# Kernel tuning notes

Hardware: AMD Instinct MI355X
Metric: run time of the kernel (lower is better)

The kernel has to match this reference:

```python
import jax, jax.numpy as jnp
import numpy as np

IN_CH = 256
OUT_CH = 128
N = 6144
ADJ_P = 0.01  # edge density -> avg degree ~61


def setup_inputs() -> dict:
    key = jax.random.key(0)
    ks = jax.random.split(key, 8)
    x = jax.random.normal(ks[0], (1, IN_CH, N), dtype=jnp.float32)
    adj = (jax.random.uniform(ks[1], (N, N)) < ADJ_P).astype(jnp.float32)
    W_fts = jax.random.normal(ks[2], (OUT_CH, IN_CH), dtype=jnp.float32) * 0.05
    w1 = jax.random.normal(ks[3], (OUT_CH,), dtype=jnp.float32) * 0.05
    b1 = jnp.zeros((1,), dtype=jnp.float32)
    w2 = jax.random.normal(ks[4], (OUT_CH,), dtype=jnp.float32) * 0.05
    b2 = jnp.zeros((1,), dtype=jnp.float32)
    vars_bias = jax.random.normal(ks[5], (1, N, OUT_CH), dtype=jnp.float32) * 0.02
    return {"x": x, "adj": adj, "W_fts": W_fts, "w1": w1, "b1": b1,
            "w2": w2, "b2": b2, "vars_bias": vars_bias}


def reference(x, adj, W_fts, w1, b1, w2, b2, vars_bias):
    # fts = Conv1d(in, out, k=1, bias=False)(x): [1, OUT_CH, N]
    fts = jnp.einsum('oi,bin->bon', W_fts, x)
    f = fts[0]  # [OUT_CH, N]
    # f1/f2 = Conv1d(out, 1, 1)(fts) -> per-node scalars [N]
    f1 = jnp.einsum('o,on->n', w1, f) + b1  # [N]
    f2 = jnp.einsum('o,on->n', w2, f) + b2  # [N]
    # scores[i,j] = leaky_relu(adj[i,j]*f1[i] + adj[i,j]*f2[j], 0.2)
    scores = jax.nn.leaky_relu(adj * f1[:, None] + adj * f2[None, :], 0.2)
    # sparse_softmax2d: per-row softmax masked to nonzero entries
    mask = (scores != 0).astype(scores.dtype)
    m = jnp.max(scores, axis=1, keepdims=True)  # stabilizer; cancels in ratio
    exps = jnp.exp(scores - m) * mask
    coefs = exps / jnp.sum(exps, axis=1, keepdims=True)  # [N, N]
    # vals = coefs @ fts.T : [N, OUT_CH]
    vals = coefs @ f.T
    # add bias, permute to [1, OUT_CH, N]
    ret = jnp.transpose(vals[None, :, :] + vars_bias, (0, 2, 1))
    return ret
```

## Files before the change

kernel.cpp:

```cpp
#include <hip/hip_runtime.h>

#define NN  6144
#define ICH 256
#define OCH 128
#define WPB 4
#define NWIN 6
#define QCAP 256

__global__ __launch_bounds__(256) void k_fts(const float* __restrict__ x,
        const float* __restrict__ W, const float* __restrict__ w1,
        const float* __restrict__ w2, float* __restrict__ ft,
        float* __restrict__ f1, float* __restrict__ f2) {
    __shared__ float xs[32][32];
    __shared__ float Ws[32][OCH + 4];
    const int n0  = blockIdx.x * 32;
    const int tid = threadIdx.x;
    const int oq = (tid & 31) * 4;
    const int nq = (tid >> 5) * 4;
    float acc[4][4] = {};
    for (int k0 = 0; k0 < ICH; k0 += 32) {
        __syncthreads();
        {
            const int nn = tid & 31;
            const int kb = tid >> 5;
#pragma unroll
            for (int r = 0; r < 4; ++r)
                xs[kb + r * 8][nn] = x[(size_t)(k0 + kb + r * 8) * NN + n0 + nn];
        }
        {
            const int kk = tid & 31;
            const int ob = tid >> 5;
#pragma unroll
            for (int r = 0; r < 16; ++r) {
                const int o = ob + r * 8;
                Ws[kk][o] = W[o * ICH + k0 + kk];
            }
        }
        __syncthreads();
#pragma unroll
        for (int kk = 0; kk < 32; ++kk) {
            const float4 xv = *(const float4*)&xs[kk][nq];
            const float4 wv = *(const float4*)&Ws[kk][oq];
            const float xa[4] = {xv.x, xv.y, xv.z, xv.w};
            const float wa[4] = {wv.x, wv.y, wv.z, wv.w};
#pragma unroll
            for (int a = 0; a < 4; ++a)
#pragma unroll
                for (int b = 0; b < 4; ++b)
                    acc[a][b] = fmaf(xa[a], wa[b], acc[a][b]);
        }
    }
#pragma unroll
    for (int a = 0; a < 4; ++a) {
        float4 v = make_float4(acc[a][0], acc[a][1], acc[a][2], acc[a][3]);
        *(float4*)&ft[(size_t)(n0 + nq + a) * OCH + oq] = v;
    }
    const float4 w1v = *(const float4*)(w1 + oq);
    const float4 w2v = *(const float4*)(w2 + oq);
    float p1[4], p2[4];
#pragma unroll
    for (int a = 0; a < 4; ++a) {
        p1[a] = acc[a][0] * w1v.x + acc[a][1] * w1v.y + acc[a][2] * w1v.z + acc[a][3] * w1v.w;
        p2[a] = acc[a][0] * w2v.x + acc[a][1] * w2v.y + acc[a][2] * w2v.z + acc[a][3] * w2v.w;
    }
#pragma unroll
    for (int m = 16; m > 0; m >>= 1) {
#pragma unroll
        for (int a = 0; a < 4; ++a) {
            p1[a] += __shfl_xor(p1[a], m);
            p2[a] += __shfl_xor(p2[a], m);
        }
    }
    if ((tid & 31) == 0) {
#pragma unroll
        for (int a = 0; a < 4; ++a) {
            f1[n0 + nq + a] = p1[a];
            f2[n0 + nq + a] = p2[a];
        }
    }
}

__global__ __launch_bounds__(256) void k_attn(const float* __restrict__ adj,
        const float* __restrict__ ft, const float* __restrict__ f1,
        const float* __restrict__ f2, const float* __restrict__ b1,
        const float* __restrict__ b2, const float* __restrict__ vb,
        float* __restrict__ out) {
    __shared__ float q_e[QCAP];
    __shared__ int   q_j[QCAP];
    __shared__ int   cnt;
    __shared__ float dpart[WPB];
    __shared__ float part[WPB][OCH];
    const int tid  = threadIdx.x;
    const int lane = tid & 63;
    const int wave = tid >> 6;
    const int i = blockIdx.x;
    if (tid == 0) cnt = 0;
    __syncthreads();
    const float s1 = f1[i] + b1[0] + b2[0];
    const float* arow = adj + (size_t)i * NN;
    const int jbase = wave * (NN / WPB) + lane * 4;
    float4 a[NWIN];
#pragma unroll
    for (int w = 0; w < NWIN; ++w)
        a[w] = *(const float4*)(arow + jbase + w * 256);
    float den = 0.f;
#pragma unroll
    for (int w = 0; w < NWIN; ++w) {
        const float4 a4 = a[w];
        const int j0 = jbase + w * 256;
        const int k = (a4.x != 0.f) + (a4.y != 0.f) + (a4.z != 0.f) + (a4.w != 0.f);
        if (k) {
            const float4 g = *(const float4*)(f2 + j0);
            int slot = atomicAdd(&cnt, k);
            if (slot + k <= QCAP) {
                if (a4.x != 0.f) { float s = s1 + g.x; s = s > 0.f ? s : 0.2f * s;
                                   float e = __expf(s); den += e; q_j[slot] = j0;     q_e[slot] = e; ++slot; }
                if (a4.y != 0.f) { float s = s1 + g.y; s = s > 0.f ? s : 0.2f * s;
                                   float e = __expf(s); den += e; q_j[slot] = j0 + 1; q_e[slot] = e; ++slot; }
                if (a4.z != 0.f) { float s = s1 + g.z; s = s > 0.f ? s : 0.2f * s;
                                   float e = __expf(s); den += e; q_j[slot] = j0 + 2; q_e[slot] = e; ++slot; }
                if (a4.w != 0.f) { float s = s1 + g.w; s = s > 0.f ? s : 0.2f * s;
                                   float e = __expf(s); den += e; q_j[slot] = j0 + 3; q_e[slot] = e; }
            }
        }
    }
#pragma unroll
    for (int off = 32; off > 0; off >>= 1) den += __shfl_xor(den, off);
    if (lane == 0) dpart[wave] = den;
    __syncthreads();
    const int nE = cnt < QCAP ? cnt : QCAP;
    float2 nm = make_float2(0.f, 0.f);
    const int c0 = 2 * lane;
    for (int idx = wave; idx < nE; idx += WPB) {
        const int   j = q_j[idx];
        const float e = q_e[idx];
        const float2 g = *(const float2*)(ft + (size_t)j * OCH + c0);
        nm.x = fmaf(e, g.x, nm.x);
        nm.y = fmaf(e, g.y, nm.y);
    }
    part[wave][c0]     = nm.x;
    part[wave][c0 + 1] = nm.y;
    __syncthreads();
    if (tid < OCH) {
        const float d   = dpart[0] + dpart[1] + dpart[2] + dpart[3];
        const float inv = 1.f / d;
        const float v = part[0][tid] + part[1][tid] + part[2][tid] + part[3][tid];
        out[(size_t)tid * NN + i] = fmaf(v, inv, vb[(size_t)i * OCH + tid]);
    }
}

extern "C" void kernel_launch(void* const* d_in, const int* in_sizes, int n_in,
                              void* d_out, int out_size, void* d_ws, size_t ws_size,
                              hipStream_t stream) {
    const float* x   = (const float*)d_in[0];
    const float* adj = (const float*)d_in[1];
    const float* W   = (const float*)d_in[2];
    const float* w1  = (const float*)d_in[3];
    const float* b1  = (const float*)d_in[4];
    const float* w2  = (const float*)d_in[5];
    const float* b2  = (const float*)d_in[6];
    const float* vb  = (const float*)d_in[7];
    float* out = (float*)d_out;

    char* ws = (char*)d_ws;
    float* ft = (float*)ws;
    float* f1 = (float*)(ws + 3145728);
    float* f2 = (float*)(ws + 3145728 + 24576);

    k_fts<<<dim3(NN / 32), 256, 0, stream>>>(x, W, w1, w2, ft, f1, f2);
    k_attn<<<dim3(NN), 256, 0, stream>>>(adj, ft, f1, f2, b1, b2, vb, out);
}
```

Baseline: 272.3 us.

## Assign one adjacency row per wavefront with double-buffered nontemporal loads

The attention kernel now maps one row to each 64-lane wavefront, so a 256-thread block covers four rows, instead of one row per block. This removes block-wide barriers and the cross-wave partial reductions. Adjacency loads are nontemporal and double-buffered in 1536-element chunks to keep more memory traffic in flight. The gather now uses float4 over two half-waves joined by a shuffle. The per-row edge queue capacity drops to 160, which could silently drop edges on denser rows. The uncoalesced transposed output stores remain.

```diff
diff --git a/kernel.cpp b/kernel.cpp
--- a/kernel.cpp
+++ b/kernel.cpp
@@ -3,9 +3,9 @@
 #define NN  6144
 #define ICH 256
 #define OCH 128
-#define WPB 4
-#define NWIN 6
-#define QCAP 256
+#define QW  160
+
+typedef float vf4 __attribute__((ext_vector_type(4)));
 
 __global__ __launch_bounds__(256) void k_fts(const float* __restrict__ x,
         const float* __restrict__ W, const float* __restrict__ w1,
@@ -85,67 +85,81 @@
         const float* __restrict__ f2, const float* __restrict__ b1,
         const float* __restrict__ b2, const float* __restrict__ vb,
         float* __restrict__ out) {
-    __shared__ float q_e[QCAP];
-    __shared__ int   q_j[QCAP];
-    __shared__ int   cnt;
-    __shared__ float dpart[WPB];
-    __shared__ float part[WPB][OCH];
+    __shared__ float q_e[4][QW];
+    __shared__ int   q_j[4][QW];
+    __shared__ int   qc[4];
     const int tid  = threadIdx.x;
     const int lane = tid & 63;
     const int wave = tid >> 6;
-    const int i = blockIdx.x;
-    if (tid == 0) cnt = 0;
-    __syncthreads();
+    const int i = blockIdx.x * 4 + wave;
+    if (lane == 0) qc[wave] = 0;
     const float s1 = f1[i] + b1[0] + b2[0];
     const float* arow = adj + (size_t)i * NN;
-    const int jbase = wave * (NN / WPB) + lane * 4;
-    float4 a[NWIN];
+    float den = 0.f;
+    vf4 ab[2][6];
 #pragma unroll
-    for (int w = 0; w < NWIN; ++w)
-        a[w] = *(const float4*)(arow + jbase + w * 256);
-    float den = 0.f;
+    for (int w = 0; w < 6; ++w)
+        ab[0][w] = __builtin_nontemporal_load((const vf4*)(arow + lane * 4 + w * 256));
 #pragma unroll
-    for (int w = 0; w < NWIN; ++w) {
-        const float4 a4 = a[w];
-        const int j0 = jbase + w * 256;
-        const int k = (a4.x != 0.f) + (a4.y != 0.f) + (a4.z != 0.f) + (a4.w != 0.f);
-        if (k) {
-            const float4 g = *(const float4*)(f2 + j0);
-            int slot = atomicAdd(&cnt, k);
-            if (slot + k <= QCAP) {
-                if (a4.x != 0.f) { float s = s1 + g.x; s = s > 0.f ? s : 0.2f * s;
-                                   float e = __expf(s); den += e; q_j[slot] = j0;     q_e[slot] = e; ++slot; }
-                if (a4.y != 0.f) { float s = s1 + g.y; s = s > 0.f ? s : 0.2f * s;
-                                   float e = __expf(s); den += e; q_j[slot] = j0 + 1; q_e[slot] = e; ++slot; }
-                if (a4.z != 0.f) { float s = s1 + g.z; s = s > 0.f ? s : 0.2f * s;
-                                   float e = __expf(s); den += e; q_j[slot] = j0 + 2; q_e[slot] = e; ++slot; }
-                if (a4.w != 0.f) { float s = s1 + g.w; s = s > 0.f ? s : 0.2f * s;
-                                   float e = __expf(s); den += e; q_j[slot] = j0 + 3; q_e[slot] = e; }
+    for (int b = 0; b < 4; ++b) {
+        if (b < 3) {
+#pragma unroll
+            for (int w = 0; w < 6; ++w)
+                ab[(b + 1) & 1][w] = __builtin_nontemporal_load(
+                    (const vf4*)(arow + (b + 1) * 1536 + lane * 4 + w * 256));
+        }
+#pragma unroll
+        for (int w = 0; w < 6; ++w) {
+            const vf4 a4 = ab[b & 1][w];
+            const int j0 = b * 1536 + w * 256 + lane * 4;
+            const int k = (a4.x != 0.f) + (a4.y != 0.f) + (a4.z != 0.f) + (a4.w != 0.f);
+            if (k) {
+                const float4 g = *(const float4*)(f2 + j0);
+                int slot = atomicAdd(&qc[wave], k);
+                if (slot + k <= QW) {
+                    if (a4.x != 0.f) { float s = s1 + g.x; s = s > 0.f ? s : 0.2f * s;
+                                       float e = __expf(s); den += e;
+                                       q_j[wave][slot] = j0;     q_e[wave][slot] = e; ++slot; }
+                    if (a4.y != 0.f) { float s = s1 + g.y; s = s > 0.f ? s : 0.2f * s;
+                                       float e = __expf(s); den += e;
+                                       q_j[wave][slot] = j0 + 1; q_e[wave][slot] = e; ++slot; }
+                    if (a4.z != 0.f) { float s = s1 + g.z; s = s > 0.f ? s : 0.2f * s;
+                                       float e = __expf(s); den += e;
+                                       q_j[wave][slot] = j0 + 2; q_e[wave][slot] = e; ++slot; }
+                    if (a4.w != 0.f) { float s = s1 + g.w; s = s > 0.f ? s : 0.2f * s;
+                                       float e = __expf(s); den += e;
+                                       q_j[wave][slot] = j0 + 3; q_e[wave][slot] = e; }
+                }
             }
         }
     }
 #pragma unroll
     for (int off = 32; off > 0; off >>= 1) den += __shfl_xor(den, off);
-    if (lane == 0) dpart[wave] = den;
-    __syncthreads();
-    const int nE = cnt < QCAP ? cnt : QCAP;
-    float2 nm = make_float2(0.f, 0.f);
-    const int c0 = 2 * lane;
-    for (int idx = wave; idx < nE; idx += WPB) {
-        const int   j = q_j[idx];
-        const float e = q_e[idx];
-        const float2 g = *(const float2*)(ft + (size_t)j * OCH + c0);
+    const float inv = 1.f / den;
+    const int nE = qc[wave] < QW ? qc[wave] : QW;
+    const int half = lane >> 5;
+    const int c0 = (lane & 31) * 4;
+    float4 nm = make_float4(0.f, 0.f, 0.f, 0.f);
+#pragma unroll 2
+    for (int idx = half; idx < nE; idx += 2) {
+        const int   j = q_j[wave][idx];
+        const float e = q_e[wave][idx];
+        const float4 g = *(const float4*)(ft + (size_t)j * OCH + c0);
         nm.x = fmaf(e, g.x, nm.x);
         nm.y = fmaf(e, g.y, nm.y);
+        nm.z = fmaf(e, g.z, nm.z);
+        nm.w = fmaf(e, g.w, nm.w);
     }
-    part[wave][c0]     = nm.x;
-    part[wave][c0 + 1] = nm.y;
-    __syncthreads();
-    if (tid < OCH) {
-        const float d   = dpart[0] + dpart[1] + dpart[2] + dpart[3];
-        const float inv = 1.f / d;
-        const float v = part[0][tid] + part[1][tid] + part[2][tid] + part[3][tid];
-        out[(size_t)tid * NN + i] = fmaf(v, inv, vb[(size_t)i * OCH + tid]);
+    nm.x += __shfl_xor(nm.x, 32);
+    nm.y += __shfl_xor(nm.y, 32);
+    nm.z += __shfl_xor(nm.z, 32);
+    nm.w += __shfl_xor(nm.w, 32);
+    if (half == 0) {
+        const float4 bv = *(const float4*)(vb + (size_t)i * OCH + c0);
+        out[(size_t)(c0    ) * NN + i] = fmaf(nm.x, inv, bv.x);
+        out[(size_t)(c0 + 1) * NN + i] = fmaf(nm.y, inv, bv.y);
+        out[(size_t)(c0 + 2) * NN + i] = fmaf(nm.z, inv, bv.z);
+        out[(size_t)(c0 + 3) * NN + i] = fmaf(nm.w, inv, bv.w);
     }
 }
 
@@ -168,5 +182,5 @@
     float* f2 = (float*)(ws + 3145728 + 24576);
 
     k_fts<<<dim3(NN / 32), 256, 0, stream>>>(x, W, w1, w2, ft, f1, f2);
-    k_attn<<<dim3(NN), 256, 0, stream>>>(adj, ft, f1, f2, b1, b2, vb, out);
+    k_attn<<<dim3(NN / 4), 256, 0, stream>>>(adj, ft, f1, f2, b1, b2, vb, out);
 }
```

New measurement: 261.4 us. 1.04x faster.

## Split attention row scan across blocks with ballot-driven gather and separate normalize kernel

Applied to the files above, without the earlier changes.

Each row's adjacency scan is split across six blocks, each covering a 1024-column window with one float4 per lane. Nonzero lanes are found with a wave ballot and their exp values are broadcast by shuffle, replacing the shared-memory atomic queue. Partial numerators and denominators go to a workspace and are reduced by a new normalize kernel, which also transposes through shared memory for coalesced output stores. The aim is more memory-level parallelism on the adj read and no atomics, at the cost of about 19 MB of partial writes and reads plus an extra launch.

```diff
diff --git a/kernel.cpp b/kernel.cpp
--- a/kernel.cpp
+++ b/kernel.cpp
@@ -3,9 +3,8 @@
 #define NN  6144
 #define ICH 256
 #define OCH 128
-#define WPB 4
-#define NWIN 6
-#define QCAP 256
+#define WPR 6
+#define GW  4
 
 __global__ __launch_bounds__(256) void k_fts(const float* __restrict__ x,
         const float* __restrict__ W, const float* __restrict__ w1,
@@ -80,72 +79,92 @@
     }
 }
 
-__global__ __launch_bounds__(256) void k_attn(const float* __restrict__ adj,
+__global__ __launch_bounds__(256) void k_scan(const float* __restrict__ adj,
         const float* __restrict__ ft, const float* __restrict__ f1,
         const float* __restrict__ f2, const float* __restrict__ b1,
-        const float* __restrict__ b2, const float* __restrict__ vb,
-        float* __restrict__ out) {
-    __shared__ float q_e[QCAP];
-    __shared__ int   q_j[QCAP];
-    __shared__ int   cnt;
-    __shared__ float dpart[WPB];
-    __shared__ float part[WPB][OCH];
+        const float* __restrict__ b2, float* __restrict__ pnum,
+        float* __restrict__ pden) {
+    __shared__ float part[GW][OCH];
+    __shared__ float pd[GW];
     const int tid  = threadIdx.x;
     const int lane = tid & 63;
     const int wave = tid >> 6;
-    const int i = blockIdx.x;
-    if (tid == 0) cnt = 0;
-    __syncthreads();
+    const int i   = blockIdx.x / WPR;
+    const int g   = blockIdx.x % WPR;
+    const int win = g * GW + wave;
+    const int j0  = win * 256 + lane * 4;
     const float s1 = f1[i] + b1[0] + b2[0];
-    const float* arow = adj + (size_t)i * NN;
-    const int jbase = wave * (NN / WPB) + lane * 4;
-    float4 a[NWIN];
-#pragma unroll
-    for (int w = 0; w < NWIN; ++w)
-        a[w] = *(const float4*)(arow + jbase + w * 256);
-    float den = 0.f;
-#pragma unroll
-    for (int w = 0; w < NWIN; ++w) {
-        const float4 a4 = a[w];
-        const int j0 = jbase + w * 256;
-        const int k = (a4.x != 0.f) + (a4.y != 0.f) + (a4.z != 0.f) + (a4.w != 0.f);
-        if (k) {
-            const float4 g = *(const float4*)(f2 + j0);
-            int slot = atomicAdd(&cnt, k);
-            if (slot + k <= QCAP) {
-                if (a4.x != 0.f) { float s = s1 + g.x; s = s > 0.f ? s : 0.2f * s;
-                                   float e = __expf(s); den += e; q_j[slot] = j0;     q_e[slot] = e; ++slot; }
-                if (a4.y != 0.f) { float s = s1 + g.y; s = s > 0.f ? s : 0.2f * s;
-                                   float e = __expf(s); den += e; q_j[slot] = j0 + 1; q_e[slot] = e; ++slot; }
-                if (a4.z != 0.f) { float s = s1 + g.z; s = s > 0.f ? s : 0.2f * s;
-                                   float e = __expf(s); den += e; q_j[slot] = j0 + 2; q_e[slot] = e; ++slot; }
-                if (a4.w != 0.f) { float s = s1 + g.w; s = s > 0.f ? s : 0.2f * s;
-                                   float e = __expf(s); den += e; q_j[slot] = j0 + 3; q_e[slot] = e; }
-            }
-        }
+    const float4 a4 = *(const float4*)(adj + (size_t)i * NN + j0);
+    float e0 = 0.f, e1 = 0.f, e2 = 0.f, e3 = 0.f, den = 0.f;
+    const bool any = (a4.x != 0.f) || (a4.y != 0.f) ||
+                     (a4.z != 0.f) || (a4.w != 0.f);
+    if (any) {
+        const float4 gg = *(const float4*)(f2 + j0);
+        if (a4.x != 0.f) { float s = s1 + gg.x; s = s > 0.f ? s : 0.2f * s; e0 = __expf(s); den += e0; }
+        if (a4.y != 0.f) { float s = s1 + gg.y; s = s > 0.f ? s : 0.2f * s; e1 = __expf(s); den += e1; }
+        if (a4.z != 0.f) { float s = s1 + gg.z; s = s > 0.f ? s : 0.2f * s; e2 = __expf(s); den += e2; }
+        if (a4.w != 0.f) { float s = s1 + gg.w; s = s > 0.f ? s : 0.2f * s; e3 = __expf(s); den += e3; }
+    }
+    unsigned long long m = __ballot(any);
+    float2 nm = make_float2(0.f, 0.f);
+    const int c0 = 2 * lane;
+    while (m) {
+        const int le = __builtin_ctzll(m);
+        m &= m - 1;
+        const float v0 = __shfl(e0, le);
+        const float v1 = __shfl(e1, le);
+        const float v2 = __shfl(e2, le);
+        const float v3 = __shfl(e3, le);
+        const int jb = win * 256 + le * 4;
+        if (v0 != 0.f) { const float2 g2 = *(const float2*)(ft + (size_t)(jb    ) * OCH + c0);
+                         nm.x = fmaf(v0, g2.x, nm.x); nm.y = fmaf(v0, g2.y, nm.y); }
+        if (v1 != 0.f) { const float2 g2 = *(const float2*)(ft + (size_t)(jb + 1) * OCH + c0);
+                         nm.x = fmaf(v1, g2.x, nm.x); nm.y = fmaf(v1, g2.y, nm.y); }
+        if (v2 != 0.f) { const float2 g2 = *(const float2*)(ft + (size_t)(jb + 2) * OCH + c0);
+                         nm.x = fmaf(v2, g2.x, nm.x); nm.y = fmaf(v2, g2.y, nm.y); }
+        if (v3 != 0.f) { const float2 g2 = *(const float2*)(ft + (size_t)(jb + 3) * OCH + c0);
+                         nm.x = fmaf(v3, g2.x, nm.x); nm.y = fmaf(v3, g2.y, nm.y); }
     }
 #pragma unroll
     for (int off = 32; off > 0; off >>= 1) den += __shfl_xor(den, off);
-    if (lane == 0) dpart[wave] = den;
-    __syncthreads();
-    const int nE = cnt < QCAP ? cnt : QCAP;
-    float2 nm = make_float2(0.f, 0.f);
-    const int c0 = 2 * lane;
-    for (int idx = wave; idx < nE; idx += WPB) {
-        const int   j = q_j[idx];
-        const float e = q_e[idx];
-        const float2 g = *(const float2*)(ft + (size_t)j * OCH + c0);
-        nm.x = fmaf(e, g.x, nm.x);
-        nm.y = fmaf(e, g.y, nm.y);
-    }
     part[wave][c0]     = nm.x;
     part[wave][c0 + 1] = nm.y;
+    if (lane == 0) pd[wave] = den;
     __syncthreads();
     if (tid < OCH) {
-        const float d   = dpart[0] + dpart[1] + dpart[2] + dpart[3];
-        const float inv = 1.f / d;
-        const float v = part[0][tid] + part[1][tid] + part[2][tid] + part[3][tid];
-        out[(size_t)tid * NN + i] = fmaf(v, inv, vb[(size_t)i * OCH + tid]);
+        const float s = part[0][tid] + part[1][tid] + part[2][tid] + part[3][tid];
+        pnum[((size_t)i * WPR + g) * OCH + tid] = s;
+        if (tid == 0) pden[i * WPR + g] = pd[0] + pd[1] + pd[2] + pd[3];
+    }
+}
+
+__global__ __launch_bounds__(256) void k_norm(const float* __restrict__ pnum,
+        const float* __restrict__ pden, const float* __restrict__ vb,
+        float* __restrict__ out) {
+    __shared__ float tile[OCH][64 + 1];
+    __shared__ float dinv[64];
+    const int tid = threadIdx.x;
+    const int i0  = blockIdx.x * 64;
+    if (tid < 64) {
+        const float* dp = pden + (size_t)(i0 + tid) * WPR;
+        dinv[tid] = 1.f / (dp[0] + dp[1] + dp[2] + dp[3] + dp[4] + dp[5]);
+    }
+    __syncthreads();
+    const int ch = tid & 127;
+    const int r0 = tid >> 7;
+    for (int rr = 0; rr < 64; rr += 2) {
+        const int r = rr + r0;
+        const float* np = pnum + ((size_t)(i0 + r) * WPR) * OCH + ch;
+        const float s = np[0] + np[OCH] + np[2 * OCH] + np[3 * OCH]
+                      + np[4 * OCH] + np[5 * OCH];
+        tile[ch][r] = fmaf(s, dinv[r], vb[(size_t)(i0 + r) * OCH + ch]);
+    }
+    __syncthreads();
+    for (int w = 0; w < 32; ++w) {
+        const int idx = w * 256 + tid;
+        const int c2  = idx >> 6;
+        const int ii  = idx & 63;
+        out[(size_t)c2 * NN + i0 + ii] = tile[c2][ii];
     }
 }
 
@@ -163,10 +182,13 @@
     float* out = (float*)d_out;
 
     char* ws = (char*)d_ws;
-    float* ft = (float*)ws;
-    float* f1 = (float*)(ws + 3145728);
-    float* f2 = (float*)(ws + 3145728 + 24576);
+    float* ft   = (float*)ws;
+    float* f1   = (float*)(ws + 3145728);
+    float* f2   = (float*)(ws + 3145728 + 24576);
+    float* pnum = (float*)(ws + 3194880);
+    float* pden = (float*)(ws + 3194880 + 18874368);
 
     k_fts<<<dim3(NN / 32), 256, 0, stream>>>(x, W, w1, w2, ft, f1, f2);
-    k_attn<<<dim3(NN), 256, 0, stream>>>(adj, ft, f1, f2, b1, b2, vb, out);
+    k_scan<<<dim3(NN * WPR), 256, 0, stream>>>(adj, ft, f1, f2, b1, b2, pnum, pden);
+    k_norm<<<dim3(NN / 64), 256, 0, stream>>>(pnum, pden, vb, out);
 }
```

Result: slower. 292.8 us (+7.5%).
